# Performance work log

Hardware: AMD Instinct MI355X
Metric: run time of the kernel (lower is better)

The kernel has to match this reference:

```python
import jax, jax.numpy as jnp
import numpy as np

CP, NP_, P = 32, 512, 2_000_000


def _grid_sample(plane, coords):
    """Bilinear grid_sample, align_corners=True, zeros padding.
    plane: [C,H,W]; coords: [P,2] in [-1,1] with (x->W, y->H). Returns [P,C]."""
    C, H, W = plane.shape
    x = (coords[:, 0] + 1.0) * 0.5 * (W - 1)
    y = (coords[:, 1] + 1.0) * 0.5 * (H - 1)
    x0 = jnp.floor(x)
    y0 = jnp.floor(y)
    wx1 = x - x0
    wy1 = y - y0

    def corner(xf, yf, w):
        xi = xf.astype(jnp.int32)
        yi = yf.astype(jnp.int32)
        valid = ((xi >= 0) & (xi < W) & (yi >= 0) & (yi < H)).astype(plane.dtype)
        xc = jnp.clip(xi, 0, W - 1)
        yc = jnp.clip(yi, 0, H - 1)
        return plane[:, yc, xc] * (w * valid)[None, :]  # [C,P]

    out = (corner(x0, y0, (1.0 - wx1) * (1.0 - wy1))
           + corner(x0 + 1.0, y0, wx1 * (1.0 - wy1))
           + corner(x0, y0 + 1.0, (1.0 - wx1) * wy1)
           + corner(x0 + 1.0, y0 + 1.0, wx1 * wy1))
    return out.T  # [P,C]


def setup_inputs() -> dict:
    key = jax.random.key(0)
    ks = jax.random.split(key, 9)
    rng, shift = 0.4, 0.1
    coordinates = jax.random.uniform(ks[0], (1, P, 3), jnp.float32, -1.0, 1.0)
    p0 = jax.random.uniform(ks[1], (CP, NP_, NP_), jnp.float32) * rng + shift
    p1 = jax.random.uniform(ks[2], (CP, NP_, NP_), jnp.float32) * rng + shift
    p2 = jax.random.uniform(ks[3], (CP, NP_, NP_), jnp.float32) * rng + shift
    W1 = jax.random.uniform(ks[4], (CP, 128), jnp.float32, -1.0, 1.0) / np.sqrt(CP)
    b1 = jax.random.uniform(ks[5], (128,), jnp.float32, -1.0, 1.0) / np.sqrt(CP)
    W2 = jax.random.uniform(ks[6], (128, 1), jnp.float32, -1.0, 1.0) / np.sqrt(128)
    b2 = jax.random.uniform(ks[7], (1,), jnp.float32, -1.0, 1.0) / np.sqrt(128)
    return {"coordinates": coordinates, "p0": p0, "p1": p1, "p2": p2,
            "W1": W1, "b1": b1, "W2": W2, "b2": b2}


def reference(coordinates, p0, p1, p2, W1, b1, W2, b2):
    c = coordinates[0]  # [P,3] (batch fixed at 1, matching plane batch)
    xy = _grid_sample(p0, c[:, 0:2])
    yz = _grid_sample(p1, c[:, 1:3])
    xz = _grid_sample(p2, c[:, ::2])
    feats = xy * yz * xz  # [P,Cp]
    h = jax.nn.relu(feats)
    h = jax.nn.relu(h @ W1 + b1)
    out = h @ W2 + b2  # [P,1]
    return out[None]  # [1,P,1]
```

## Files before the change

### kernel.cpp

```cpp
#include <hip/hip_runtime.h>
#include <hip/hip_fp16.h>
#include <cstdint>
#include <cstddef>

#define HH 512
#define WW 512
#define PLANE_H2 (512 * 512 * 16)
#define PLANE_BYTES (1 << 24)
#define NTILE (3 * 512 * 8)
#define NBKT 64

typedef _Float16 f16x8 __attribute__((ext_vector_type(8)));
typedef float    f32x4 __attribute__((ext_vector_type(4)));

__device__ __forceinline__ int key_of(float x, float y, float z) {
    int qx = min(max((int)((x + 1.0f) * 255.5f), 0), 511) >> 7;
    int qy = min(max((int)((y + 1.0f) * 255.5f), 0), 511) >> 7;
    int qz = min(max((int)((z + 1.0f) * 255.5f), 0), 511) >> 7;
    return ((qx >> 1) << 5) | ((qy >> 1) << 4) | ((qz >> 1) << 3) |
           ((qx & 1) << 2) | ((qy & 1) << 1) | (qz & 1);
}

__device__ __forceinline__ float4 ldco(const float4* __restrict__ sc,
                                       int g, int pl15, int P, int nG) {
    int gg = min(g, nG - 1);
    int pc = min((gg << 4) + pl15, P - 1);
    return sc[pc];
}

__device__ __forceinline__ void issue_slot(const char* __restrict__ trb,
                                           float4 cc, int kb,
                                           float* wx, float* wy, f16x8* q) {
    float cx = cc.x, cy = cc.y, cz = cc.z;
#pragma unroll
    for (int pl = 0; pl < 3; ++pl) {
        float u = (pl == 1) ? cy : cx;
        float v = (pl == 0) ? cy : cz;
        float xf = (u + 1.0f) * (0.5f * 511.0f);
        float yf = (v + 1.0f) * (0.5f * 511.0f);
        float x0f = floorf(xf), y0f = floorf(yf);
        wx[pl] = xf - x0f;
        wy[pl] = yf - y0f;
        int x0 = min(max((int)x0f, 0), 510);
        int y0 = min(max((int)y0f, 0), 510);
        const char* bp = trb + ((size_t)pl * PLANE_BYTES) +
                         ((size_t)(y0 * WW + x0) * 64 + kb * 16);
        q[pl * 4 + 0] = *(const f16x8*)(bp);
        q[pl * 4 + 1] = *(const f16x8*)(bp + 64);
        q[pl * 4 + 2] = *(const f16x8*)(bp + WW * 64);
        q[pl * 4 + 3] = *(const f16x8*)(bp + WW * 64 + 64);
    }
}

__device__ __forceinline__ void compute_store(
    const f16x8* q, const float* wx, const float* wy, float ccw,
    const _Float16* __restrict__ W1h,
    const float* b1r, const float* w2r, float b2v,
    float* __restrict__ out, int kb, int pl15) {
    float s[8];
#pragma unroll
    for (int pl = 0; pl < 3; ++pl) {
        float w11 = wx[pl] * wy[pl];
        float w01 = wx[pl] - w11;
        float w10 = wy[pl] - w11;
        float w00 = 1.0f - wx[pl] - w10;
#pragma unroll
        for (int e = 0; e < 8; ++e) {
            float smp = (float)q[pl * 4 + 0][e] * w00 + (float)q[pl * 4 + 1][e] * w01 +
                        (float)q[pl * 4 + 2][e] * w10 + (float)q[pl * 4 + 3][e] * w11;
            s[e] = (pl == 0) ? smp : s[e] * smp;
        }
    }
    f16x8 af;
#pragma unroll
    for (int e = 0; e < 8; ++e) af[e] = (_Float16)fmaxf(s[e], 0.0f);

    float sum0 = 0.f, sum1 = 0.f, sum2 = 0.f, sum3 = 0.f;
#pragma unroll
    for (int hf = 0; hf < 2; ++hf) {
        f32x4 a0 = {0.f, 0.f, 0.f, 0.f}, a1 = a0, a2 = a0, a3 = a0;
        int ntb = hf * 4;
        const f16x8* bp0 = (const f16x8*)&W1h[(16 * (ntb + 0) + pl15) * 40 + kb * 8];
        const f16x8* bp1 = (const f16x8*)&W1h[(16 * (ntb + 1) + pl15) * 40 + kb * 8];
        const f16x8* bp2 = (const f16x8*)&W1h[(16 * (ntb + 2) + pl15) * 40 + kb * 8];
        const f16x8* bp3 = (const f16x8*)&W1h[(16 * (ntb + 3) + pl15) * 40 + kb * 8];
        a0 = __builtin_amdgcn_mfma_f32_16x16x32_f16(af, *bp0, a0, 0, 0, 0);
        a1 = __builtin_amdgcn_mfma_f32_16x16x32_f16(af, *bp1, a1, 0, 0, 0);
        a2 = __builtin_amdgcn_mfma_f32_16x16x32_f16(af, *bp2, a2, 0, 0, 0);
        a3 = __builtin_amdgcn_mfma_f32_16x16x32_f16(af, *bp3, a3, 0, 0, 0);
#pragma unroll
        for (int r = 0; r < 4; ++r) {
            float h0 = fmaxf(a0[r] + b1r[ntb + 0], 0.0f);
            float h1 = fmaxf(a1[r] + b1r[ntb + 1], 0.0f);
            float h2 = fmaxf(a2[r] + b1r[ntb + 2], 0.0f);
            float h3 = fmaxf(a3[r] + b1r[ntb + 3], 0.0f);
            float v4 = h0 * w2r[ntb + 0] + h1 * w2r[ntb + 1] +
                       h2 * w2r[ntb + 2] + h3 * w2r[ntb + 3];
            if (r == 0) sum0 += v4;
            else if (r == 1) sum1 += v4;
            else if (r == 2) sum2 += v4;
            else sum3 += v4;
        }
    }
#pragma unroll
    for (int m = 1; m <= 8; m <<= 1) {
        sum0 += __shfl_xor(sum0, m, 64);
        sum1 += __shfl_xor(sum1, m, 64);
        sum2 += __shfl_xor(sum2, m, 64);
        sum3 += __shfl_xor(sum3, m, 64);
    }
    int sb = (kb << 4) + kb * 4;
    int i0 = __float_as_int(__shfl(ccw, sb + 0, 64));
    int i1 = __float_as_int(__shfl(ccw, sb + 1, 64));
    int i2 = __float_as_int(__shfl(ccw, sb + 2, 64));
    int i3 = __float_as_int(__shfl(ccw, sb + 3, 64));
    if (pl15 == 0) {
        out[i0] = sum0 + b2v;
        out[i1] = sum1 + b2v;
        out[i2] = sum2 + b2v;
        out[i3] = sum3 + b2v;
    }
}

__device__ __forceinline__ void dev_barrier(unsigned int* ctr, int nb, int t) {
    __syncthreads();
    if (t == 0) {
        __threadfence();
        __hip_atomic_fetch_add(ctr, 1u, __ATOMIC_ACQ_REL, __HIP_MEMORY_SCOPE_AGENT);
        long long t0 = wall_clock64();
        while (__hip_atomic_load(ctr, __ATOMIC_ACQUIRE, __HIP_MEMORY_SCOPE_AGENT)
               < (unsigned)nb) {
            __builtin_amdgcn_s_sleep(8);
            if (wall_clock64() - t0 > 50000000LL) break;
        }
        __threadfence();
    }
    __syncthreads();
}

__global__ __launch_bounds__(256, 3) void kp_main(
    const float* __restrict__ coords,
    const float* __restrict__ p0, const float* __restrict__ p1,
    const float* __restrict__ p2,
    const float* __restrict__ W1, const float* __restrict__ b1,
    const float* __restrict__ W2, const float* __restrict__ b2,
    float* __restrict__ out, int P,
    unsigned int* __restrict__ bar, unsigned int* __restrict__ hist,
    int* __restrict__ blkhist, float4* __restrict__ sc,
    __half2* __restrict__ tr)
{
    __shared__ __align__(16) char smem[10240];
    float    (*tileF)[65] = (float(*)[65])smem;
    _Float16* W1h         = (_Float16*)smem;
    __shared__ int hcnt[NBKT];
    __shared__ int hl_pref[NBKT];
    __shared__ int psum4[4 * NBKT];
    __shared__ int lcur[NBKT];
    int t  = threadIdx.x;
    int nb = gridDim.x;

    for (int bid = blockIdx.x; bid < NTILE; bid += nb) {
        int xb = bid & 7, y = (bid >> 3) & 511, pl = bid >> 12;
        const float* src = (pl == 0) ? p0 : ((pl == 1) ? p1 : p2);
        int xbase = xb * 64;
        __syncthreads();
        int x = t & 63, cq = t >> 6;
#pragma unroll
        for (int i = 0; i < 8; ++i) {
            int c = cq * 8 + i;
            tileF[c][x] = src[c * (HH * WW) + y * WW + xbase + x];
        }
        __syncthreads();
        int c2 = t & 15, xq = t >> 4;
        __half2* dst = tr + (size_t)pl * PLANE_H2 + ((size_t)y * WW + xbase) * 16;
#pragma unroll
        for (int i = 0; i < 4; ++i) {
            int xx = xq * 4 + i;
            dst[xx * 16 + c2] =
                __floats2half2_rn(tileF[2 * c2][xx], tileF[2 * c2 + 1][xx]);
        }
    }

    if (t < NBKT) hcnt[t] = 0;
    __syncthreads();
    int nCh = (P + 255) >> 8;
    for (int ch = blockIdx.x; ch < nCh; ch += nb) {
        int i = (ch << 8) + t;
        if (i < P) {
            float x = coords[3 * i], y = coords[3 * i + 1], z = coords[3 * i + 2];
            atomicAdd(&hcnt[key_of(x, y, z)], 1);
        }
    }
    __syncthreads();
    if (t < NBKT) {
        blkhist[blockIdx.x * NBKT + t] = hcnt[t];
        atomicAdd(&hist[t], (unsigned)hcnt[t]);
    }

    dev_barrier(&bar[0], nb, t);

    if (t < NBKT) hl_pref[t] = (int)hist[t];
    __syncthreads();
    int pref = 0;
    if (t < NBKT)
        for (int k = 0; k < t; ++k) pref += hl_pref[k];
    {
        int key = t & (NBKT - 1), q = t >> 6;
        int lo = (int)(((long long)q * blockIdx.x) >> 2);
        int hi = (int)(((long long)(q + 1) * blockIdx.x) >> 2);
        int sacc = 0;
        for (int b = lo; b < hi; ++b) sacc += blkhist[b * NBKT + key];
        psum4[t] = sacc;
    }
    __syncthreads();
    if (t < NBKT)
        lcur[t] = pref + psum4[t] + psum4[NBKT + t] +
                  psum4[2 * NBKT + t] + psum4[3 * NBKT + t];
    __syncthreads();

    for (int ch = blockIdx.x; ch < nCh; ch += nb) {
        int i = (ch << 8) + t;
        if (i < P) {
            float x = coords[3 * i], y = coords[3 * i + 1], z = coords[3 * i + 2];
            int slot = atomicAdd(&lcur[key_of(x, y, z)], 1);
            float4 v = {x, y, z, __int_as_float(i)};
            sc[slot] = v;
        }
    }

    __syncthreads();
    for (int e = t; e < 4096; e += 256) {
        int j = e >> 5, k = e & 31;
        W1h[j * 40 + k] = (_Float16)W1[k * 128 + j];
    }

    dev_barrier(&bar[16], nb, t);

    int wave = t >> 6, lane = t & 63;
    int pl15 = lane & 15;
    int kb   = lane >> 4;
    const char* trb = (const char*)tr;

    float b1r[8], w2r[8];
#pragma unroll
    for (int nt = 0; nt < 8; ++nt) {
        b1r[nt] = b1[16 * nt + pl15];
        w2r[nt] = W2[16 * nt + pl15];
    }
    float b2v = b2[0];

    int nG  = (P + 15) >> 4;
    int xcd = blockIdx.x & 7;
    int lb  = blockIdx.x >> 3;
    int nbs = (nb >> 3) + ((blockIdx.x & 7) < (nb & 7) ? 1 : 0);
    int gs  = (int)(((long long)xcd * nG) >> 3);
    int ge  = (int)(((long long)(xcd + 1) * nG) >> 3);
    int nws = nbs * 4;

    float wxA[3], wyA[3], wxB[3], wyB[3];
    f16x8 qA[12], qB[12];

    int g = gs + lb * 4 + wave;
    if (g < ge) {
        float4 cc0 = ldco(sc, g, pl15, P, nG);
        float4 cc1 = ldco(sc, g + nws, pl15, P, nG);
        issue_slot(trb, cc0, kb, wxA, wyA, qA);
        float cwA = cc0.w, cwB;
        while (true) {
            issue_slot(trb, cc1, kb, wxB, wyB, qB);
            cwB = cc1.w;
            cc0 = ldco(sc, g + 2 * nws, pl15, P, nG);
            compute_store(qA, wxA, wyA, cwA, W1h, b1r, w2r, b2v, out, kb, pl15);
            g += nws;
            if (g >= ge) break;

            issue_slot(trb, cc0, kb, wxA, wyA, qA);
            cwA = cc0.w;
            cc1 = ldco(sc, g + 2 * nws, pl15, P, nG);
            compute_store(qB, wxB, wyB, cwB, W1h, b1r, w2r, b2v, out, kb, pl15);
            g += nws;
            if (g >= ge) break;
        }
    }
}

__global__ __launch_bounds__(256) void kp_direct(
    const float* __restrict__ coords,
    const float* __restrict__ p0, const float* __restrict__ p1,
    const float* __restrict__ p2,
    const float* __restrict__ W1, const float* __restrict__ b1,
    const float* __restrict__ W2, const float* __restrict__ b2,
    float* __restrict__ out, int P)
{
    __shared__ float feats[256][33];
    int t = threadIdx.x;
    int wave = t >> 6, lane = t & 63, c = lane & 31, xsel = lane >> 5;
    int pbase = blockIdx.x * 256;

    for (int i = 0; i < 64; ++i) {
        int p = pbase + i * 4 + wave;
        if (p < P) {
            float cx = coords[3 * p + 0];
            float cy = coords[3 * p + 1];
            float cz = coords[3 * p + 2];
            float f = 1.0f;
#pragma unroll
            for (int pl = 0; pl < 3; ++pl) {
                const float* plane = (pl == 0) ? p0 : ((pl == 1) ? p1 : p2);
                float u = (pl == 1) ? cy : cx;
                float v = (pl == 0) ? cy : cz;
                float xf = (u + 1.0f) * (0.5f * 511.0f);
                float yf = (v + 1.0f) * (0.5f * 511.0f);
                float x0f = floorf(xf), y0f = floorf(yf);
                float wx = xf - x0f, wy = yf - y0f;
                int x0 = min(max((int)x0f, 0), 510);
                int y0 = min(max((int)y0f, 0), 510);
                const float* bp = plane + (size_t)c * (HH * WW) +
                                  (size_t)y0 * WW + (x0 + xsel);
                float v0 = bp[0];
                float v1 = bp[WW];
                float wxl = xsel ? wx : (1.0f - wx);
                float sm = (v0 * (1.0f - wy) + v1 * wy) * wxl;
                sm += __shfl_xor(sm, 32, 64);
                f *= sm;
            }
            if (xsel == 0) feats[i * 4 + wave][c] = fmaxf(f, 0.0f);
        }
    }
    __syncthreads();
    int p = pbase + t;
    if (p < P) {
        float fr[32];
#pragma unroll
        for (int k = 0; k < 32; ++k) fr[k] = feats[t][k];
        float acc = b2[0];
#pragma unroll 4
        for (int j = 0; j < 128; ++j) {
            float a = b1[j];
#pragma unroll
            for (int k = 0; k < 32; ++k) a += fr[k] * W1[k * 128 + j];
            acc += fmaxf(a, 0.0f) * W2[j];
        }
        out[p] = acc;
    }
}

extern "C" void kernel_launch(void* const* d_in, const int* in_sizes, int n_in,
                              void* d_out, int out_size, void* d_ws, size_t ws_size,
                              hipStream_t stream) {
    const float* coords = (const float*)d_in[0];
    const float* p0 = (const float*)d_in[1];
    const float* p1 = (const float*)d_in[2];
    const float* p2 = (const float*)d_in[3];
    const float* W1 = (const float*)d_in[4];
    const float* b1 = (const float*)d_in[5];
    const float* W2 = (const float*)d_in[6];
    const float* b2 = (const float*)d_in[7];
    float* out = (float*)d_out;
    int P = in_sizes[0] / 3;

    const size_t bh_off = 512;
    const size_t sc_off = bh_off + 1024 * NBKT * sizeof(int);
    const size_t tr_off = (sc_off + (size_t)P * 16 + 255) & ~(size_t)255;
    const size_t need   = tr_off + (size_t)3 * PLANE_BYTES;

    if (ws_size >= need) {
        int dev = 0, nCU = 0, maxb = 0;
        hipGetDevice(&dev);
        hipDeviceGetAttribute(&nCU, hipDeviceAttributeMultiprocessorCount, dev);
        hipOccupancyMaxActiveBlocksPerMultiprocessor(&maxb, kp_main, 256, 0);
        if (nCU <= 0) nCU = 32;
        if (maxb <= 0) maxb = 1;
        int nblk = nCU * maxb;
        if (nblk > 1024) nblk = 1024;

        unsigned int* bar  = (unsigned int*)d_ws;
        unsigned int* hist = (unsigned int*)((char*)d_ws + 256);
        int*          bh   = (int*)((char*)d_ws + bh_off);
        float4*       sc   = (float4*)((char*)d_ws + sc_off);
        __half2*      tr   = (__half2*)((char*)d_ws + tr_off);
        hipMemsetAsync(d_ws, 0, 512, stream);
        kp_main<<<dim3(nblk), dim3(256), 0, stream>>>(
            coords, p0, p1, p2, W1, b1, W2, b2, out, P, bar, hist, bh, sc, tr);
    } else {
        int nblk = (P + 255) / 256;
        kp_direct<<<dim3(nblk), dim3(256), 0, stream>>>(
            coords, p0, p1, p2, W1, b1, W2, b2, out, P);
    }
}
```

Measured before the change: 443.3 us.

## Refine spatial sort to 4096 Morton buckets with global atomic cursors

Increases the coordinate bucketing from 64 coarse buckets to 4096 Morton-ordered buckets (16 cells per axis), so points processed together are much closer in space and their plane gathers hit cache better. The per-block histogram and prefix-sum scheme is replaced: each block computes a full exclusive scan of the global histogram in shared memory, and slots are assigned via global atomic cursors per bucket. This adds global atomic traffic and a larger memset, and makes the order within a bucket nondeterministic.

New measurement: 530.8 us. 19.7% more time.

```diff
diff --git a/kernel.cpp b/kernel.cpp
--- a/kernel.cpp
+++ b/kernel.cpp
@@ -8,17 +8,23 @@
 #define PLANE_H2 (512 * 512 * 16)
 #define PLANE_BYTES (1 << 24)
 #define NTILE (3 * 512 * 8)
-#define NBKT 64
+#define NBKT 4096
 
 typedef _Float16 f16x8 __attribute__((ext_vector_type(8)));
 typedef float    f32x4 __attribute__((ext_vector_type(4)));
 
 __device__ __forceinline__ int key_of(float x, float y, float z) {
-    int qx = min(max((int)((x + 1.0f) * 255.5f), 0), 511) >> 7;
-    int qy = min(max((int)((y + 1.0f) * 255.5f), 0), 511) >> 7;
-    int qz = min(max((int)((z + 1.0f) * 255.5f), 0), 511) >> 7;
-    return ((qx >> 1) << 5) | ((qy >> 1) << 4) | ((qz >> 1) << 3) |
-           ((qx & 1) << 2) | ((qy & 1) << 1) | (qz & 1);
+    int qx = min(max((int)((x + 1.0f) * 255.5f), 0), 511) >> 5;
+    int qy = min(max((int)((y + 1.0f) * 255.5f), 0), 511) >> 5;
+    int qz = min(max((int)((z + 1.0f) * 255.5f), 0), 511) >> 5;
+    int k = 0;
+#pragma unroll
+    for (int b = 0; b < 4; ++b) {
+        k |= ((qx >> b) & 1) << (3 * b + 2);
+        k |= ((qy >> b) & 1) << (3 * b + 1);
+        k |= ((qz >> b) & 1) << (3 * b + 0);
+    }
+    return k;
 }
 
 __device__ __forceinline__ float4 ldco(const float4* __restrict__ sc,
@@ -146,16 +152,14 @@
     const float* __restrict__ W2, const float* __restrict__ b2,
     float* __restrict__ out, int P,
     unsigned int* __restrict__ bar, unsigned int* __restrict__ hist,
-    int* __restrict__ blkhist, float4* __restrict__ sc,
+    unsigned int* __restrict__ cur, float4* __restrict__ sc,
     __half2* __restrict__ tr)
 {
-    __shared__ __align__(16) char smem[10240];
+    __shared__ __align__(16) char smem[16384];
     float    (*tileF)[65] = (float(*)[65])smem;
+    int*      ihist       = (int*)smem;
     _Float16* W1h         = (_Float16*)smem;
-    __shared__ int hcnt[NBKT];
-    __shared__ int hl_pref[NBKT];
-    __shared__ int psum4[4 * NBKT];
-    __shared__ int lcur[NBKT];
+    __shared__ int spart[256];
     int t  = threadIdx.x;
     int nb = gridDim.x;
 
@@ -180,55 +184,62 @@
                 __floats2half2_rn(tileF[2 * c2][xx], tileF[2 * c2 + 1][xx]);
         }
     }
-
-    if (t < NBKT) hcnt[t] = 0;
+    __syncthreads();
+
+    for (int e = t; e < NBKT; e += 256) ihist[e] = 0;
     __syncthreads();
     int nCh = (P + 255) >> 8;
     for (int ch = blockIdx.x; ch < nCh; ch += nb) {
         int i = (ch << 8) + t;
         if (i < P) {
             float x = coords[3 * i], y = coords[3 * i + 1], z = coords[3 * i + 2];
-            atomicAdd(&hcnt[key_of(x, y, z)], 1);
-        }
-    }
-    __syncthreads();
-    if (t < NBKT) {
-        blkhist[blockIdx.x * NBKT + t] = hcnt[t];
-        atomicAdd(&hist[t], (unsigned)hcnt[t]);
-    }
+            atomicAdd(&ihist[key_of(x, y, z)], 1);
+        }
+    }
+    __syncthreads();
+    for (int e = t; e < NBKT; e += 256)
+        if (ihist[e]) atomicAdd(&hist[e], (unsigned)ihist[e]);
 
     dev_barrier(&bar[0], nb, t);
 
-    if (t < NBKT) hl_pref[t] = (int)hist[t];
-    __syncthreads();
-    int pref = 0;
-    if (t < NBKT)
-        for (int k = 0; k < t; ++k) pref += hl_pref[k];
     {
-        int key = t & (NBKT - 1), q = t >> 6;
-        int lo = (int)(((long long)q * blockIdx.x) >> 2);
-        int hi = (int)(((long long)(q + 1) * blockIdx.x) >> 2);
-        int sacc = 0;
-        for (int b = lo; b < hi; ++b) sacc += blkhist[b * NBKT + key];
-        psum4[t] = sacc;
-    }
-    __syncthreads();
-    if (t < NBKT)
-        lcur[t] = pref + psum4[t] + psum4[NBKT + t] +
-                  psum4[2 * NBKT + t] + psum4[3 * NBKT + t];
+        int acc = 0;
+#pragma unroll
+        for (int k = 0; k < 16; ++k) {
+            int h = (int)hist[t * 16 + k];
+            ihist[t * 16 + k] = h;
+            acc += h;
+        }
+        spart[t] = acc;
+        __syncthreads();
+        for (int off = 1; off < 256; off <<= 1) {
+            int v = (t >= off) ? spart[t - off] : 0;
+            __syncthreads();
+            spart[t] += v;
+            __syncthreads();
+        }
+        int run = (t > 0) ? spart[t - 1] : 0;
+#pragma unroll
+        for (int k = 0; k < 16; ++k) {
+            int h = ihist[t * 16 + k];
+            ihist[t * 16 + k] = run;
+            run += h;
+        }
+    }
     __syncthreads();
 
     for (int ch = blockIdx.x; ch < nCh; ch += nb) {
         int i = (ch << 8) + t;
         if (i < P) {
             float x = coords[3 * i], y = coords[3 * i + 1], z = coords[3 * i + 2];
-            int slot = atomicAdd(&lcur[key_of(x, y, z)], 1);
+            int key  = key_of(x, y, z);
+            int slot = ihist[key] + (int)atomicAdd(&cur[key], 1u);
             float4 v = {x, y, z, __int_as_float(i)};
             sc[slot] = v;
         }
     }
-
-    __syncthreads();
+    __syncthreads();
+
     for (int e = t; e < 4096; e += 256) {
         int j = e >> 5, k = e & 31;
         W1h[j * 40 + k] = (_Float16)W1[k * 128 + j];
@@ -359,10 +370,12 @@
     float* out = (float*)d_out;
     int P = in_sizes[0] / 3;
 
-    const size_t bh_off = 512;
-    const size_t sc_off = bh_off + 1024 * NBKT * sizeof(int);
-    const size_t tr_off = (sc_off + (size_t)P * 16 + 255) & ~(size_t)255;
-    const size_t need   = tr_off + (size_t)3 * PLANE_BYTES;
+    const size_t hist_off = 256;
+    const size_t cur_off  = hist_off + NBKT * sizeof(unsigned int);
+    const size_t sc_off   = (cur_off + NBKT * sizeof(unsigned int) + 255) & ~(size_t)255;
+    const size_t tr_off   = (sc_off + (size_t)P * 16 + 255) & ~(size_t)255;
+    const size_t need     = tr_off + (size_t)3 * PLANE_BYTES;
+    const size_t zero_len = sc_off;
 
     if (ws_size >= need) {
         int dev = 0, nCU = 0, maxb = 0;
@@ -372,16 +385,15 @@
         if (nCU <= 0) nCU = 32;
         if (maxb <= 0) maxb = 1;
         int nblk = nCU * maxb;
-        if (nblk > 1024) nblk = 1024;
 
         unsigned int* bar  = (unsigned int*)d_ws;
-        unsigned int* hist = (unsigned int*)((char*)d_ws + 256);
-        int*          bh   = (int*)((char*)d_ws + bh_off);
+        unsigned int* hist = (unsigned int*)((char*)d_ws + hist_off);
+        unsigned int* cur  = (unsigned int*)((char*)d_ws + cur_off);
         float4*       sc   = (float4*)((char*)d_ws + sc_off);
         __half2*      tr   = (__half2*)((char*)d_ws + tr_off);
-        hipMemsetAsync(d_ws, 0, 512, stream);
+        hipMemsetAsync(d_ws, 0, zero_len, stream);
         kp_main<<<dim3(nblk), dim3(256), 0, stream>>>(
-            coords, p0, p1, p2, W1, b1, W2, b2, out, P, bar, hist, bh, sc, tr);
+            coords, p0, p1, p2, W1, b1, W2, b2, out, P, bar, hist, cur, sc, tr);
     } else {
         int nblk = (P + 255) / 256;
         kp_direct<<<dim3(nblk), dim3(256), 0, stream>>>(
```
